# Kernel optimization log

Measured on AMD Instinct MI355X. Metric: run time of the kernel, lower is better.

## Reference

```python
import jax, jax.numpy as jnp
import numpy as np

VOXEL_SIZE = (0.1, 0.1, 0.2)
PC_RANGE = (-51.2, -51.2, -5.0, 51.2, 51.2, 3.0)
B, N, C = 8, 1_000_000, 4


def setup_inputs() -> dict:
    key = jax.random.key(0)
    u = jax.random.uniform(key, (B, N, C), dtype=jnp.float32)
    # xyz spread slightly beyond the point-cloud range so some points are out-of-range;
    # 4th channel is an intensity in [0, 1].
    lo = jnp.array([-60.0, -60.0, -8.0, 0.0], jnp.float32)
    hi = jnp.array([60.0, 60.0, 6.0, 1.0], jnp.float32)
    pts = lo + u * (hi - lo)
    # inject NaNs to exercise the not_nan_mask path
    pts = pts.at[:, ::1000, 0].set(jnp.nan)
    return {"points": pts}


def reference(points):
    # Padded/masked equivalent of DynamicVoxelizer.forward.
    # Instead of stream-compacting each batch (dynamic shapes), we return
    # fixed-shape [B, N, ...] arrays plus a validity mask; invalid entries
    # carry the same sentinel (-1 coords / -1 idx) the torch code filters on.
    vs = jnp.array(VOXEL_SIZE, dtype=points.dtype)          # (3,) x,y,z
    rng = jnp.array(PC_RANGE, dtype=points.dtype)           # (6,)
    pmin = rng[:3]
    grid = jnp.round((rng[3:] - rng[:3]) / vs).astype(jnp.int32)  # (nx, ny, nz)

    xyz = points[..., :3]                                   # [B, N, 3]
    not_nan = ~jnp.isnan(points).any(axis=-1)               # [B, N]

    # dynamic voxelization (mmcv semantics, max_num_points=-1):
    # per-point integer voxel coordinate, -1 sentinel if out of grid.
    cf = jnp.floor((xyz - pmin) / vs)                       # [B, N, 3] float (x,y,z order)
    c = cf.astype(jnp.int32)
    in_range = ((c >= 0) & (c < grid)).all(axis=-1)         # [B, N]
    valid = not_nan & in_range                              # [B, N]

    # voxelizer returns coords in (z, y, x) order; -1 where invalid
    voxel_coords = jnp.where(valid[..., None], c[..., ::-1], -1)

    # _get_point_offsets: reorder zyx->xyz, center = coord*vs + min + vs/2
    centers = cf * vs + pmin + vs * 0.5                     # [B, N, 3]
    point_offsets = jnp.where(valid[..., None], xyz - centers, 0.0)

    point_idxes = jnp.where(valid, jnp.arange(N, dtype=jnp.int32)[None, :], -1)
    points_out = jnp.where(valid[..., None], points, 0.0)

    return points_out, voxel_coords, point_idxes, point_offsets, valid
```

## Files before the change

### kernel.cpp

```cpp
#include <hip/hip_runtime.h>


#define NPTS 1000000
#define BLK 256

typedef float f4 __attribute__((ext_vector_type(4)));

__global__ __launch_bounds__(BLK) void voxelize_kernel(
    const f4* __restrict__ pts, float* __restrict__ out, int total) {
  __shared__ __align__(16) float s_vox[BLK * 3];
  __shared__ __align__(16) float s_poff[BLK * 3];
  __shared__ __align__(16) float s_misc[BLK * 2];

  const int tid  = threadIdx.x;
  const int base = blockIdx.x * BLK;
  const int i    = base + tid;

  f4 p = __builtin_nontemporal_load(&pts[i]);

  bool has_nan = (p.x != p.x) | (p.y != p.y) | (p.z != p.z) | (p.w != p.w);

  float fx = floorf((p.x - (-51.2f)) / 0.1f);
  float fy = floorf((p.y - (-51.2f)) / 0.1f);
  float fz = floorf((p.z - (-5.0f))  / 0.2f);
  int cx = (int)fx, cy = (int)fy, cz = (int)fz;

  bool in_range = (cx >= 0) & (cx < 1024) &
                  (cy >= 0) & (cy < 1024) &
                  (cz >= 0) & (cz < 40);
  bool valid = (!has_nan) && in_range;

  float ox = p.x - (fx * 0.1f + (-51.2f) + 0.05f);
  float oy = p.y - (fy * 0.1f + (-51.2f) + 0.05f);
  float oz = p.z - (fz * 0.2f + (-5.0f)  + 0.1f);

  f4 po = valid ? p : (f4){0.0f, 0.0f, 0.0f, 0.0f};
  ((f4*)out)[i] = po;

  if (valid) {
    s_vox[tid * 3 + 0] = (float)cz;
    s_vox[tid * 3 + 1] = (float)cy;
    s_vox[tid * 3 + 2] = (float)cx;
    s_poff[tid * 3 + 0] = ox;
    s_poff[tid * 3 + 1] = oy;
    s_poff[tid * 3 + 2] = oz;
    s_misc[tid]       = (float)(i % NPTS);
    s_misc[BLK + tid] = 1.0f;
  } else {
    s_vox[tid * 3 + 0] = -1.0f;
    s_vox[tid * 3 + 1] = -1.0f;
    s_vox[tid * 3 + 2] = -1.0f;
    s_poff[tid * 3 + 0] = 0.0f;
    s_poff[tid * 3 + 1] = 0.0f;
    s_poff[tid * 3 + 2] = 0.0f;
    s_misc[tid]       = -1.0f;
    s_misc[BLK + tid] = 0.0f;
  }
  __syncthreads();

  const long long t = total;
  f4* gvox  = (f4*)(out + 4 * t  + (long long)base * 3);
  f4* gpoff = (f4*)(out + 8 * t  + (long long)base * 3);
  f4* gidx  = (f4*)(out + 7 * t  + base);
  f4* gval  = (f4*)(out + 11 * t + base);

  const f4* v4 = (const f4*)s_vox;
  const f4* o4 = (const f4*)s_poff;
  const f4* m4 = (const f4*)s_misc;

  if (tid < 192) {
    gvox[tid]  = v4[tid];
    gpoff[tid] = o4[tid];
  } else {
    int j = tid - 192;
    gidx[j] = m4[j];
    gval[j] = m4[64 + j];
  }
}

__global__ __launch_bounds__(64) void voxelize_tail(
    const float* __restrict__ ptsf, float* __restrict__ out, int total, int start) {
  int i = start + blockIdx.x * blockDim.x + threadIdx.x;
  if (i >= total) return;
  float px = ptsf[i * 4 + 0], py = ptsf[i * 4 + 1];
  float pz = ptsf[i * 4 + 2], pw = ptsf[i * 4 + 3];
  bool has_nan = (px != px) | (py != py) | (pz != pz) | (pw != pw);
  float fx = floorf((px - (-51.2f)) / 0.1f);
  float fy = floorf((py - (-51.2f)) / 0.1f);
  float fz = floorf((pz - (-5.0f))  / 0.2f);
  int cx = (int)fx, cy = (int)fy, cz = (int)fz;
  bool in_range = (cx >= 0) & (cx < 1024) & (cy >= 0) & (cy < 1024) &
                  (cz >= 0) & (cz < 40);
  bool valid = (!has_nan) && in_range;
  float ox = px - (fx * 0.1f + (-51.2f) + 0.05f);
  float oy = py - (fy * 0.1f + (-51.2f) + 0.05f);
  float oz = pz - (fz * 0.2f + (-5.0f)  + 0.1f);
  long long t = total;
  out[i * 4 + 0] = valid ? px : 0.0f;
  out[i * 4 + 1] = valid ? py : 0.0f;
  out[i * 4 + 2] = valid ? pz : 0.0f;
  out[i * 4 + 3] = valid ? pw : 0.0f;
  float* vox  = out + 4 * t  + (long long)i * 3;
  float* poff = out + 8 * t  + (long long)i * 3;
  if (valid) {
    vox[0] = (float)cz; vox[1] = (float)cy; vox[2] = (float)cx;
    poff[0] = ox; poff[1] = oy; poff[2] = oz;
    out[7 * t + i]  = (float)(i % NPTS);
    out[11 * t + i] = 1.0f;
  } else {
    vox[0] = -1.0f; vox[1] = -1.0f; vox[2] = -1.0f;
    poff[0] = 0.0f; poff[1] = 0.0f; poff[2] = 0.0f;
    out[7 * t + i]  = -1.0f;
    out[11 * t + i] = 0.0f;
  }
}

extern "C" void kernel_launch(void* const* d_in, const int* in_sizes, int n_in,
                              void* d_out, int out_size, void* d_ws, size_t ws_size,
                              hipStream_t stream) {
  (void)n_in; (void)d_ws; (void)ws_size; (void)out_size;
  const f4* pts = (const f4*)d_in[0];
  float* out = (float*)d_out;
  int total = in_sizes[0] / 4;
  int full_blocks = total / BLK;
  if (full_blocks > 0)
    voxelize_kernel<<<full_blocks, BLK, 0, stream>>>(pts, out, total);
  int rem = total - full_blocks * BLK;
  if (rem > 0)
    voxelize_tail<<<(rem + 63) / 64, 64, 0, stream>>>((const float*)d_in[0], out,
                                                      total, full_blocks * BLK);
}
```

Baseline: 450.1 us.

## Give each wave 256 points with four loads in flight and wave-local staging

Each 64-lane wave now handles a contiguous chunk of 256 points. Every lane issues four nontemporal float4 loads up front, then stages its voxel coords, offsets, indices and mask in a per-wave LDS region. The block-wide __syncthreads is replaced by a wave barrier, and each wave writes its own coalesced float4 output rows. The goal is more memory-level parallelism per thread and less block synchronization in a bandwidth-bound kernel. The cost is more registers per thread and fewer blocks in flight.

```diff
diff --git a/kernel.cpp b/kernel.cpp
--- a/kernel.cpp
+++ b/kernel.cpp
@@ -2,80 +2,82 @@
 
 
 #define NPTS 1000000
-#define BLK 256
+#define BLK 128
+#define WPT 256
 
 typedef float f4 __attribute__((ext_vector_type(4)));
 
 __global__ __launch_bounds__(BLK) void voxelize_kernel(
     const f4* __restrict__ pts, float* __restrict__ out, int total) {
-  __shared__ __align__(16) float s_vox[BLK * 3];
-  __shared__ __align__(16) float s_poff[BLK * 3];
-  __shared__ __align__(16) float s_misc[BLK * 2];
+  __shared__ __align__(16) float s_vox [2][WPT * 3];
+  __shared__ __align__(16) float s_poff[2][WPT * 3];
+  __shared__ __align__(16) float s_misc[2][WPT * 2];
 
-  const int tid  = threadIdx.x;
-  const int base = blockIdx.x * BLK;
-  const int i    = base + tid;
+  const int lane  = threadIdx.x & 63;
+  const int wave  = threadIdx.x >> 6;
+  const int pbase = blockIdx.x * ((BLK / 64) * WPT) + wave * WPT;
 
-  f4 p = __builtin_nontemporal_load(&pts[i]);
+  f4 p[4];
+#pragma unroll
+  for (int k = 0; k < 4; ++k)
+    p[k] = __builtin_nontemporal_load(&pts[pbase + k * 64 + lane]);
 
-  bool has_nan = (p.x != p.x) | (p.y != p.y) | (p.z != p.z) | (p.w != p.w);
+  float* sv = s_vox[wave];
+  float* so = s_poff[wave];
+  float* sm = s_misc[wave];
 
-  float fx = floorf((p.x - (-51.2f)) / 0.1f);
-  float fy = floorf((p.y - (-51.2f)) / 0.1f);
-  float fz = floorf((p.z - (-5.0f))  / 0.2f);
-  int cx = (int)fx, cy = (int)fy, cz = (int)fz;
+#pragma unroll
+  for (int k = 0; k < 4; ++k) {
+    const int i = pbase + k * 64 + lane;
+    f4 q = p[k];
+    bool has_nan = (q.x != q.x) | (q.y != q.y) | (q.z != q.z) | (q.w != q.w);
 
-  bool in_range = (cx >= 0) & (cx < 1024) &
-                  (cy >= 0) & (cy < 1024) &
-                  (cz >= 0) & (cz < 40);
-  bool valid = (!has_nan) && in_range;
+    float fx = floorf((q.x - (-51.2f)) / 0.1f);
+    float fy = floorf((q.y - (-51.2f)) / 0.1f);
+    float fz = floorf((q.z - (-5.0f))  / 0.2f);
+    int cx = (int)fx, cy = (int)fy, cz = (int)fz;
 
-  float ox = p.x - (fx * 0.1f + (-51.2f) + 0.05f);
-  float oy = p.y - (fy * 0.1f + (-51.2f) + 0.05f);
-  float oz = p.z - (fz * 0.2f + (-5.0f)  + 0.1f);
+    bool in_range = (cx >= 0) & (cx < 1024) &
+                    (cy >= 0) & (cy < 1024) &
+                    (cz >= 0) & (cz < 40);
+    bool valid = (!has_nan) && in_range;
 
-  f4 po = valid ? p : (f4){0.0f, 0.0f, 0.0f, 0.0f};
-  ((f4*)out)[i] = po;
+    float ox = q.x - (fx * 0.1f + (-51.2f) + 0.05f);
+    float oy = q.y - (fy * 0.1f + (-51.2f) + 0.05f);
+    float oz = q.z - (fz * 0.2f + (-5.0f)  + 0.1f);
 
-  if (valid) {
-    s_vox[tid * 3 + 0] = (float)cz;
-    s_vox[tid * 3 + 1] = (float)cy;
-    s_vox[tid * 3 + 2] = (float)cx;
-    s_poff[tid * 3 + 0] = ox;
-    s_poff[tid * 3 + 1] = oy;
-    s_poff[tid * 3 + 2] = oz;
-    s_misc[tid]       = (float)(i % NPTS);
-    s_misc[BLK + tid] = 1.0f;
-  } else {
-    s_vox[tid * 3 + 0] = -1.0f;
-    s_vox[tid * 3 + 1] = -1.0f;
-    s_vox[tid * 3 + 2] = -1.0f;
-    s_poff[tid * 3 + 0] = 0.0f;
-    s_poff[tid * 3 + 1] = 0.0f;
-    s_poff[tid * 3 + 2] = 0.0f;
-    s_misc[tid]       = -1.0f;
-    s_misc[BLK + tid] = 0.0f;
+    f4 po = valid ? q : (f4){0.0f, 0.0f, 0.0f, 0.0f};
+    ((f4*)out)[i] = po;
+
+    const int s = k * 64 + lane;
+    sv[s * 3 + 0] = valid ? (float)cz : -1.0f;
+    sv[s * 3 + 1] = valid ? (float)cy : -1.0f;
+    sv[s * 3 + 2] = valid ? (float)cx : -1.0f;
+    so[s * 3 + 0] = valid ? ox : 0.0f;
+    so[s * 3 + 1] = valid ? oy : 0.0f;
+    so[s * 3 + 2] = valid ? oz : 0.0f;
+    sm[s]       = valid ? (float)(i % NPTS) : -1.0f;
+    sm[WPT + s] = valid ? 1.0f : 0.0f;
   }
-  __syncthreads();
+
+  __builtin_amdgcn_wave_barrier();
 
   const long long t = total;
-  f4* gvox  = (f4*)(out + 4 * t  + (long long)base * 3);
-  f4* gpoff = (f4*)(out + 8 * t  + (long long)base * 3);
-  f4* gidx  = (f4*)(out + 7 * t  + base);
-  f4* gval  = (f4*)(out + 11 * t + base);
+  f4* gvox  = (f4*)(out + 4  * t) + (long long)pbase * 3 / 4;
+  f4* gpoff = (f4*)(out + 8  * t) + (long long)pbase * 3 / 4;
+  f4* gidx  = (f4*)(out + 7  * t) + pbase / 4;
+  f4* gval  = (f4*)(out + 11 * t) + pbase / 4;
 
-  const f4* v4 = (const f4*)s_vox;
-  const f4* o4 = (const f4*)s_poff;
-  const f4* m4 = (const f4*)s_misc;
+  const f4* v4 = (const f4*)sv;
+  const f4* o4 = (const f4*)so;
+  const f4* m4 = (const f4*)sm;
 
-  if (tid < 192) {
-    gvox[tid]  = v4[tid];
-    gpoff[tid] = o4[tid];
-  } else {
-    int j = tid - 192;
-    gidx[j] = m4[j];
-    gval[j] = m4[64 + j];
-  }
+#pragma unroll
+  for (int j = 0; j < 3; ++j) gvox[j * 64 + lane] = v4[j * 64 + lane];
+#pragma unroll
+  for (int j = 0; j < 3; ++j) gpoff[j * 64 + lane] = o4[j * 64 + lane];
+  gidx[lane] = m4[lane];
+  gval[lane] = m4[64 + lane];
 }
 
 __global__ __launch_bounds__(64) void voxelize_tail(
@@ -122,11 +124,12 @@
   const f4* pts = (const f4*)d_in[0];
   float* out = (float*)d_out;
   int total = in_sizes[0] / 4;
-  int full_blocks = total / BLK;
+  const int ppb = (BLK / 64) * WPT;
+  int full_blocks = total / ppb;
   if (full_blocks > 0)
     voxelize_kernel<<<full_blocks, BLK, 0, stream>>>(pts, out, total);
-  int rem = total - full_blocks * BLK;
+  int rem = total - full_blocks * ppb;
   if (rem > 0)
     voxelize_tail<<<(rem + 63) / 64, 64, 0, stream>>>((const float*)d_in[0], out,
-                                                      total, full_blocks * BLK);
+                                                      total, full_blocks * ppb);
 }
```

New measurement: 451.0 us. About the same (+0.2%).
